# Kernel optimization log

Measured on AMD Instinct MI355X. Metric: run time of the kernel, lower is better.

## Reference

```python
import jax, jax.numpy as jnp
import numpy as np

FS = 512
SEQ_LEN = 16384
BATCH = 128
TAPS = 513  # common kernel length; per-band kernels zero-padded at the tail
N_BANDS = 20


def _design_kernels():
    """Windowed-sinc (fir1/firwin-style, hamming) bandpass kernels, tensorpac-like."""
    pha = [(f, f + 2.0) for f in np.arange(2.0, 22.0, 2.0)]    # 10 phase bands
    amp = [(f, f + 10.0) for f in np.arange(30.0, 130.0, 10.0)]  # 10 amp bands
    cycles = [3] * 10 + [6] * 10
    bands = pha + amp
    K = np.zeros((N_BANDS, TAPS), np.float32)
    for i, ((lo, hi), c) in enumerate(zip(bands, cycles)):
        order = min(int(c * FS / lo), TAPS - 1)  # fir_order ~ cycle * fs / low_hz
        taps = order + 1
        n = np.arange(taps) - (taps - 1) / 2.0
        f1, f2 = lo / FS, hi / FS
        h = 2.0 * f2 * np.sinc(2.0 * f2 * n) - 2.0 * f1 * np.sinc(2.0 * f1 * n)
        h *= np.hamming(taps)
        K[i, :taps] = h.astype(np.float32)
    return jnp.asarray(K)


def setup_inputs() -> dict:
    key = jax.random.key(0)
    x = jax.random.normal(key, (BATCH, 1, SEQ_LEN), dtype=jnp.float32)
    return {"x": x, "kernels": _design_kernels(), "padlen": TAPS - 1}


def _filtfilt_bands(x2d, kernels, P):
    """scipy.signal.filtfilt(b, 1.0, x, padlen=P) for all bands at once.
    x2d: (B, L); kernels: (nb, T) FIR taps. Odd-extension padding + lfilter_zi
    initial conditions (== constant extension of the first sample by T-1)."""
    B, L = x2d.shape
    nb, T = kernels.shape
    # odd extension: left_j = 2*x[0] - x[P-j], right_j = 2*x[-1] - x[-2-j]
    left = 2.0 * x2d[:, :1] - x2d[:, 1:P + 1][:, ::-1]
    right = 2.0 * x2d[:, -1:] - x2d[:, -P - 1:-1][:, ::-1]
    ext = jnp.concatenate([left, x2d, right], axis=1)  # (B, L + 2P)
    krev = kernels[:, ::-1][:, None, :]  # (nb, 1, T); correlation with b[::-1] == causal conv with b

    def causal_conv(sig, groups):
        # sig: (B, C, Ls); constant left-extension by T-1 (lfilter zi*x0 semantics)
        pad = jnp.repeat(sig[..., :1], T - 1, axis=-1)
        s = jnp.concatenate([pad, sig], axis=-1)
        return jax.lax.conv_general_dilated(
            s, krev, (1,), 'VALID',
            dimension_numbers=('NCW', 'OIW', 'NCW'),
            feature_group_count=groups)

    y = causal_conv(ext[:, None, :], 1)        # forward pass -> (B, nb, L+2P)
    y2 = causal_conv(y[:, :, ::-1], nb)        # backward pass (grouped, per-band)
    return y2[:, :, ::-1][:, :, P:P + L]       # un-reverse and trim padding


def reference(x, kernels, padlen):
    # x: (B, 1, L) -> (B, 1, n_bands, L)
    out = _filtfilt_bands(x[:, 0, :], kernels, padlen)
    return out[:, None, :, :]
```

## Files before the change

kernel.cpp:

```cpp
#include <hip/hip_runtime.h>

#define LSEQ   16384
#define NB     20
#define NBATCH 128
#define TAPS   513
#define CT     (2*TAPS - 1)
#define MAXSTEP 72

#define TT     2048
#define SPANE  3088
#define STRIDE 3096
#define EXTEND 16896
#define GMAX   17407

#define HDR_OFF  0
#define CS_OFF   4096
#define CSTRIDE  1040
#define ATAB_OFF 98304

typedef short  v8s  __attribute__((ext_vector_type(8)));
typedef __bf16 v8bf __attribute__((ext_vector_type(8)));
typedef float  v16f __attribute__((ext_vector_type(16)));

__device__ __forceinline__ unsigned short f2bf(float f) {
    union { float f; unsigned u; } v; v.f = f;
    return (unsigned short)((v.u + 0x7fffu + ((v.u >> 16) & 1u)) >> 16);
}

__device__ __forceinline__ v16f vzero() {
    v16f z;
    #pragma unroll
    for (int i = 0; i < 16; ++i) z[i] = 0.f;
    return z;
}

__global__ __launch_bounds__(512) void autoc_kernel(
    const float* __restrict__ Kg, float* __restrict__ Cs)
{
    __shared__ __align__(16) float kk4[4][520];
    __shared__ float ps[512];
    const int band = blockIdx.x, y = blockIdx.y;
    const int tid = threadIdx.x;
    const int rel = tid & 127, q = tid >> 7;
    const int d = 128 * y + rel;

    for (int j = tid; j < TAPS; j += 512) {
        float v = Kg[band * TAPS + j];
        kk4[0][j] = v;
        if (j >= 1) kk4[1][j - 1] = v;
        if (j >= 2) kk4[2][j - 2] = v;
        if (j >= 3) kk4[3][j - 3] = v;
    }
    if (tid < 40) {
        int c = tid / 10, t = tid % 10;
        int j = 510 + t;
        if (j >= TAPS - c && j < 520) kk4[c][j] = 0.f;
    }
    __syncthreads();

    float s = 0.f;
    if (d < CT) {
        int al = d - 512; if (al < 0) al = -al;
        const int n  = TAPS - al;
        const int c  = al & 3, sh4 = (al >> 2) << 2;
        const int nq = (((n + 3) >> 2) + 3) & ~3;
        int i0 = q * nq, i1 = i0 + nq; if (i1 > n) i1 = n;
        float s0 = 0.f, s1 = 0.f, s2 = 0.f, s3 = 0.f;
        int i = i0;
        for (; i + 3 < i1; i += 4) {
            float4 a = *(const float4*)&kk4[0][i];
            float4 b = *(const float4*)&kk4[c][i + sh4];
            s0 = fmaf(a.x, b.x, s0);
            s1 = fmaf(a.y, b.y, s1);
            s2 = fmaf(a.z, b.z, s2);
            s3 = fmaf(a.w, b.w, s3);
        }
        for (; i < i1; ++i) s0 = fmaf(kk4[0][i], kk4[c][i + sh4], s0);
        s = (s0 + s1) + (s2 + s3);
    }
    ps[tid] = s;
    __syncthreads();
    if (q == 0 && d < CT) {
        float tot = (ps[rel] + ps[rel + 128]) + (ps[rel + 256] + ps[rel + 384]);
        Cs[band * CSTRIDE + d] = tot;
    }
}

__global__ __launch_bounds__(1024) void table_kernel(
    const float* __restrict__ Cs, int2* __restrict__ hdr, short* __restrict__ atab)
{
    __shared__ float csh[CT];
    __shared__ int smin, smax, sk0, sN;
    const int band = blockIdx.x, tid = threadIdx.x;
    if (tid == 0) { smin = CT; smax = 0; }
    __syncthreads();

    const float* cb = Cs + band * CSTRIDE;
    int lmin = CT, lmax = 0;
    for (int j = tid; j < CT; j += 1024) {
        float v = cb[j];
        csh[j] = v;
        if (v != 0.f) { if (j < lmin) lmin = j; if (j > lmax) lmax = j; }
    }
    if (lmin < CT) atomicMin(&smin, lmin);
    if (lmax > 0)  atomicMax(&smax, lmax);
    __syncthreads();

    if (tid == 0) {
        int k0 = smin & ~15;
        int k1 = ((smax + 31) >> 4) << 4;
        int N  = (k1 - k0) / 16 + 1;
        int2 h; h.x = k0; h.y = N;
        hdr[band] = h;
        sk0 = k0; sN = N;
    }
    __syncthreads();

    const int k0 = sk0, N = sN;
    int nf = N + 3; if (nf > MAXSTEP) nf = MAXSTEP;
    for (int idx = tid; idx < nf * 64; idx += 1024) {
        int s = idx >> 6, lane = idx & 63;
        int m = lane & 31, kh = lane >> 5;
        int base = k0 + 16 * s + 8 * kh - m;
        v8s r;
        #pragma unroll
        for (int j = 0; j < 8; ++j) {
            int ci = base + j;
            float v = (ci >= 0 && ci < CT) ? csh[ci] : 0.f;
            r[j] = (short)f2bf(v);
        }
        *(v8s*)(atab + ((size_t)(band * MAXSTEP + s) * 64 + lane) * 8) = r;
    }
}

__global__ __launch_bounds__(256, 3) void filt_main(
    const float* __restrict__ x, const short* __restrict__ atab,
    const int2* __restrict__ hdr, float* __restrict__ out)
{
    __shared__ __align__(16) unsigned short extl[8 * STRIDE];
    const int tid = threadIdx.x;
    const int tile = blockIdx.x, grp = blockIdx.y, bg = blockIdx.z;
    const int T0 = tile * TT;

    const bool edge = (T0 < 512) || (T0 + SPANE > EXTEND);
    for (int b = 0; b < 8; ++b) {
        const float* xb = x + (size_t)(bg * 8 + b) * LSEQ;
        float x0 = 0.f, xN = 0.f;
        if (edge) { x0 = xb[0]; xN = xb[LSEQ - 1]; }
        for (int e4 = tid; e4 < SPANE / 4; e4 += 256) {
            const int e = 4 * e4;
            const int g0 = T0 + e;
            float v0, v1, v2, v3;
            if (g0 >= 512 && g0 + 4 <= EXTEND) {
                float4 xv = *(const float4*)(xb + (g0 - 512));
                v0 = xv.x; v1 = xv.y; v2 = xv.z; v3 = xv.w;
            } else {
                float vv[4];
                #pragma unroll
                for (int t = 0; t < 4; ++t) {
                    int g = g0 + t; if (g > GMAX) g = GMAX;
                    vv[t] = (g < 512)    ? 2.f * x0 - xb[512 - g]
                          : (g < EXTEND) ? xb[g - 512]
                          :                2.f * xN - xb[2 * LSEQ + 512 - 2 - g];
                }
                v0 = vv[0]; v1 = vv[1]; v2 = vv[2]; v3 = vv[3];
            }
            ushort4 qv = make_ushort4(f2bf(v0), f2bf(v1), f2bf(v2), f2bf(v3));
            *(ushort4*)&extl[b * STRIDE + e] = qv;
        }
    }
    __syncthreads();

    const int lane = tid & 63;
    const int w    = tid >> 6;
    const int n    = lane & 31, kh = lane >> 5;
    const int brow = n & 7,  tb = n >> 3;
    const unsigned short* bpb = extl + brow * STRIDE + 512 * w + 32 * tb + 8 * kh;

    const int g_start[6] = {0, 4, 8, 11, 15, 20};
    const int g_list[20] = {0,19,18,17, 1,16,15,14, 2,3,13, 4,5,6,12, 7,8,9,10,11};

    for (int bi = g_start[grp]; bi < g_start[grp + 1]; ++bi) {
        const int band = g_list[bi];
        const int2 hh = hdr[band];
        const int k0 = hh.x, N = hh.y;
        const unsigned short* bp = bpb + k0;
        const short* ap = atab + (size_t)(band * MAXSTEP) * 512 + lane * 8;

        v16f ac0 = vzero(), ac1 = vzero(), ac2 = vzero(), ac3 = vzero();
        v8bf A0 = __builtin_bit_cast(v8bf, *(const v8s*)ap);
        v8bf A1 = __builtin_bit_cast(v8bf, *(const v8s*)(ap + 512));
        v8bf A2 = __builtin_bit_cast(v8bf, *(const v8s*)(ap + 1024));
        v8bf B0 = *(const v8bf*)(bp);
        v8bf B1 = *(const v8bf*)(bp + 128);
        v8bf B2 = *(const v8bf*)(bp + 256);
        v8bf B3 = *(const v8bf*)(bp + 384);

        #pragma unroll 2
        for (int s = 0; s < N; ++s) {
            v8bf An  = __builtin_bit_cast(v8bf, *(const v8s*)(ap + (size_t)(s + 3) * 512));
            const unsigned short* bn = bp + 16 * (s + 1);
            v8bf Bn0 = *(const v8bf*)(bn);
            v8bf Bn1 = *(const v8bf*)(bn + 128);
            v8bf Bn2 = *(const v8bf*)(bn + 256);
            v8bf Bn3 = *(const v8bf*)(bn + 384);
            __builtin_amdgcn_s_setprio(1);
            ac0 = __builtin_amdgcn_mfma_f32_32x32x16_bf16(A0, B0, ac0, 0, 0, 0);
            ac1 = __builtin_amdgcn_mfma_f32_32x32x16_bf16(A0, B1, ac1, 0, 0, 0);
            ac2 = __builtin_amdgcn_mfma_f32_32x32x16_bf16(A0, B2, ac2, 0, 0, 0);
            ac3 = __builtin_amdgcn_mfma_f32_32x32x16_bf16(A0, B3, ac3, 0, 0, 0);
            __builtin_amdgcn_s_setprio(0);
            A0 = A1; A1 = A2; A2 = An;
            B0 = Bn0; B1 = Bn1; B2 = Bn2; B3 = Bn3;
        }

        float* ob = out + ((size_t)(bg * 8 + brow) * NB + band) * LSEQ
                        + T0 + 512 * w + 32 * tb + 4 * kh;
        #pragma unroll
        for (int q = 0; q < 4; ++q) {
            *(float4*)(ob +       8 * q) = make_float4(ac0[4*q], ac0[4*q+1], ac0[4*q+2], ac0[4*q+3]);
            *(float4*)(ob + 128 + 8 * q) = make_float4(ac1[4*q], ac1[4*q+1], ac1[4*q+2], ac1[4*q+3]);
            *(float4*)(ob + 256 + 8 * q) = make_float4(ac2[4*q], ac2[4*q+1], ac2[4*q+2], ac2[4*q+3]);
            *(float4*)(ob + 384 + 8 * q) = make_float4(ac3[4*q], ac3[4*q+1], ac3[4*q+2], ac3[4*q+3]);
        }
    }
}

extern "C" void kernel_launch(void* const* d_in, const int* in_sizes, int n_in,
                              void* d_out, int out_size, void* d_ws, size_t ws_size,
                              hipStream_t stream) {
    const float* x  = (const float*)d_in[0];
    const float* Kg = (const float*)d_in[1];
    float* out = (float*)d_out;

    char* wsb = (char*)d_ws;
    int2*  hdr  = (int2*)(wsb + HDR_OFF);
    float* Cs   = (float*)(wsb + CS_OFF);
    short* atab = (short*)(wsb + ATAB_OFF);

    autoc_kernel<<<dim3(NB, 9), dim3(512), 0, stream>>>(Kg, Cs);
    table_kernel<<<dim3(NB), dim3(1024), 0, stream>>>(Cs, hdr, atab);
    filt_main<<<dim3(LSEQ / TT, 5, NBATCH / 8), dim3(256), 0, stream>>>(x, atab, hdr, out);
}
```

Before: 223.9 us.

## Rebalance band groups, rotate band order per wave, prefetch next band operands

Regroups the 20 bands into five block groups with a new assignment meant to balance MFMA work per group. Each wave starts at a different band within its group, so waves in a block touch different atab regions and output rows at the same time. The first A/B operands for the next band are loaded before the current band's accumulators are stored, hiding the load latency at band boundaries. This adds register pressure from carrying extra operand registers across the store epilogue, which could hurt at the 3-blocks-per-SM bound.

```diff
diff --git a/kernel.cpp b/kernel.cpp
--- a/kernel.cpp
+++ b/kernel.cpp
@@ -177,44 +177,74 @@
     const int brow = n & 7,  tb = n >> 3;
     const unsigned short* bpb = extl + brow * STRIDE + 512 * w + 32 * tb + 8 * kh;
 
-    const int g_start[6] = {0, 4, 8, 11, 15, 20};
-    const int g_list[20] = {0,19,18,17, 1,16,15,14, 2,3,13, 4,5,6,12, 7,8,9,10,11};
-
-    for (int bi = g_start[grp]; bi < g_start[grp + 1]; ++bi) {
-        const int band = g_list[bi];
-        const int2 hh = hdr[band];
-        const int k0 = hh.x, N = hh.y;
-        const unsigned short* bp = bpb + k0;
-        const short* ap = atab + (size_t)(band * MAXSTEP) * 512 + lane * 8;
+    const int g_start[6] = {0, 2, 5, 8, 13, 20};
+    const int g_list[20] = {0,8, 1,4,17, 2,3,6, 5,7,9,10,14, 11,12,13,15,16,18,19};
+    const int gbeg = g_start[grp];
+    const int glen = g_start[grp + 1] - gbeg;
+    int rot = w; while (rot >= glen) rot -= glen;
+
+    int pos = rot;
+    int band = g_list[gbeg + pos];
+    int2 hh = hdr[band];
+    const unsigned short* bp = bpb + hh.x;
+    const short* ap = atab + (size_t)(band * MAXSTEP) * 512 + lane * 8;
+    int N = hh.y;
+    v8bf A0 = __builtin_bit_cast(v8bf, *(const v8s*)ap);
+    v8bf A1 = __builtin_bit_cast(v8bf, *(const v8s*)(ap + 512));
+    v8bf A2 = __builtin_bit_cast(v8bf, *(const v8s*)(ap + 1024));
+    v8bf B0 = *(const v8bf*)(bp);
+    v8bf B1 = *(const v8bf*)(bp + 128);
+    v8bf B2 = *(const v8bf*)(bp + 256);
+    v8bf B3 = *(const v8bf*)(bp + 384);
+
+    for (int j = 0; j < glen; ++j) {
+        const int curBand = band;
+        const int Nc = N;
+        const unsigned short* bpc = bp;
+        const short* apc = ap;
+        v8bf a0 = A0, a1 = A1, a2 = A2;
+        v8bf b0 = B0, b1 = B1, b2 = B2, b3 = B3;
+
+        const bool more = (j + 1 < glen);
+        if (more) {
+            pos = pos + 1; if (pos >= glen) pos -= glen;
+            band = g_list[gbeg + pos];
+            hh = hdr[band];
+            bp = bpb + hh.x;
+            ap = atab + (size_t)(band * MAXSTEP) * 512 + lane * 8;
+            N = hh.y;
+        }
 
         v16f ac0 = vzero(), ac1 = vzero(), ac2 = vzero(), ac3 = vzero();
-        v8bf A0 = __builtin_bit_cast(v8bf, *(const v8s*)ap);
-        v8bf A1 = __builtin_bit_cast(v8bf, *(const v8s*)(ap + 512));
-        v8bf A2 = __builtin_bit_cast(v8bf, *(const v8s*)(ap + 1024));
-        v8bf B0 = *(const v8bf*)(bp);
-        v8bf B1 = *(const v8bf*)(bp + 128);
-        v8bf B2 = *(const v8bf*)(bp + 256);
-        v8bf B3 = *(const v8bf*)(bp + 384);
-
         #pragma unroll 2
-        for (int s = 0; s < N; ++s) {
-            v8bf An  = __builtin_bit_cast(v8bf, *(const v8s*)(ap + (size_t)(s + 3) * 512));
-            const unsigned short* bn = bp + 16 * (s + 1);
+        for (int s = 0; s < Nc; ++s) {
+            v8bf An  = __builtin_bit_cast(v8bf, *(const v8s*)(apc + (size_t)(s + 3) * 512));
+            const unsigned short* bn = bpc + 16 * (s + 1);
             v8bf Bn0 = *(const v8bf*)(bn);
             v8bf Bn1 = *(const v8bf*)(bn + 128);
             v8bf Bn2 = *(const v8bf*)(bn + 256);
             v8bf Bn3 = *(const v8bf*)(bn + 384);
             __builtin_amdgcn_s_setprio(1);
-            ac0 = __builtin_amdgcn_mfma_f32_32x32x16_bf16(A0, B0, ac0, 0, 0, 0);
-            ac1 = __builtin_amdgcn_mfma_f32_32x32x16_bf16(A0, B1, ac1, 0, 0, 0);
-            ac2 = __builtin_amdgcn_mfma_f32_32x32x16_bf16(A0, B2, ac2, 0, 0, 0);
-            ac3 = __builtin_amdgcn_mfma_f32_32x32x16_bf16(A0, B3, ac3, 0, 0, 0);
+            ac0 = __builtin_amdgcn_mfma_f32_32x32x16_bf16(a0, b0, ac0, 0, 0, 0);
+            ac1 = __builtin_amdgcn_mfma_f32_32x32x16_bf16(a0, b1, ac1, 0, 0, 0);
+            ac2 = __builtin_amdgcn_mfma_f32_32x32x16_bf16(a0, b2, ac2, 0, 0, 0);
+            ac3 = __builtin_amdgcn_mfma_f32_32x32x16_bf16(a0, b3, ac3, 0, 0, 0);
             __builtin_amdgcn_s_setprio(0);
-            A0 = A1; A1 = A2; A2 = An;
-            B0 = Bn0; B1 = Bn1; B2 = Bn2; B3 = Bn3;
-        }
-
-        float* ob = out + ((size_t)(bg * 8 + brow) * NB + band) * LSEQ
+            a0 = a1; a1 = a2; a2 = An;
+            b0 = Bn0; b1 = Bn1; b2 = Bn2; b3 = Bn3;
+        }
+
+        if (more) {
+            A0 = __builtin_bit_cast(v8bf, *(const v8s*)ap);
+            A1 = __builtin_bit_cast(v8bf, *(const v8s*)(ap + 512));
+            A2 = __builtin_bit_cast(v8bf, *(const v8s*)(ap + 1024));
+            B0 = *(const v8bf*)(bp);
+            B1 = *(const v8bf*)(bp + 128);
+            B2 = *(const v8bf*)(bp + 256);
+            B3 = *(const v8bf*)(bp + 384);
+        }
+
+        float* ob = out + ((size_t)(bg * 8 + brow) * NB + curBand) * LSEQ
                         + T0 + 512 * w + 32 * tb + 4 * kh;
         #pragma unroll
         for (int q = 0; q < 4; ++q) {
```

After: 224.3 us. Within noise of the previous version (+0.1%).

## Reuse sliding LDS B-window registers across MFMA steps with swizzled LDS layout

Applied to the files above, without the earlier changes.

The four accumulators now cover adjacent 32-sample column blocks, so their B operands overlap by 32 samples. An 8-register rotating window of B fragments is kept, and each step issues one new LDS load where the old code issued four. The extl layout gets an XOR swizzle to reduce bank conflicts, and the band-to-block grouping is rebalanced. In exchange the loop is padded to a multiple of 8 steps, which lengthens the A-table (MAXSTEP raised to 80) and adds some zero-padded wasted MFMAs.

```diff
diff --git a/kernel.cpp b/kernel.cpp
--- a/kernel.cpp
+++ b/kernel.cpp
@@ -5,7 +5,7 @@
 #define NBATCH 128
 #define TAPS   513
 #define CT     (2*TAPS - 1)
-#define MAXSTEP 72
+#define MAXSTEP 80
 
 #define TT     2048
 #define SPANE  3088
@@ -32,6 +32,11 @@
     #pragma unroll
     for (int i = 0; i < 16; ++i) z[i] = 0.f;
     return z;
+}
+
+__device__ __forceinline__ v8bf ld_swz(const unsigned short* base, int ldw) {
+    int ph = ldw ^ (((ldw >> 6) & 3) << 2);
+    return __builtin_bit_cast(v8bf, *(const v8s*)((const char*)base + (size_t)ph * 4));
 }
 
 __global__ __launch_bounds__(512) void autoc_kernel(
@@ -117,7 +122,8 @@
     __syncthreads();
 
     const int k0 = sk0, N = sN;
-    int nf = N + 3; if (nf > MAXSTEP) nf = MAXSTEP;
+    const int Np = (N + 7) & ~7;
+    int nf = Np + 3; if (nf > MAXSTEP) nf = MAXSTEP;
     for (int idx = tid; idx < nf * 64; idx += 1024) {
         int s = idx >> 6, lane = idx & 63;
         int m = lane & 31, kh = lane >> 5;
@@ -166,7 +172,9 @@
                 v0 = vv[0]; v1 = vv[1]; v2 = vv[2]; v3 = vv[3];
             }
             ushort4 qv = make_ushort4(f2bf(v0), f2bf(v1), f2bf(v2), f2bf(v3));
-            *(ushort4*)&extl[b * STRIDE + e] = qv;
+            int ldw = (b * STRIDE + e) >> 1;
+            int ph  = ldw ^ (((ldw >> 6) & 3) << 2);
+            *(ushort4*)((char*)extl + (size_t)ph * 4) = qv;
         }
     }
     __syncthreads();
@@ -175,53 +183,54 @@
     const int w    = tid >> 6;
     const int n    = lane & 31, kh = lane >> 5;
     const int brow = n & 7,  tb = n >> 3;
-    const unsigned short* bpb = extl + brow * STRIDE + 512 * w + 32 * tb + 8 * kh;
-
-    const int g_start[6] = {0, 4, 8, 11, 15, 20};
-    const int g_list[20] = {0,19,18,17, 1,16,15,14, 2,3,13, 4,5,6,12, 7,8,9,10,11};
+    const int laneDW = brow * (STRIDE / 2) + 256 * w + 64 * tb + 4 * kh;
+
+    const int g_start[6] = {0, 2, 5, 8, 14, 20};
+    const int g_list[20] = {0,5, 1,4,14, 2,3,6, 7,8,9,10,15,16, 11,12,13,17,18,19};
 
     for (int bi = g_start[grp]; bi < g_start[grp + 1]; ++bi) {
         const int band = g_list[bi];
         const int2 hh = hdr[band];
         const int k0 = hh.x, N = hh.y;
-        const unsigned short* bp = bpb + k0;
+        const int Np   = (N + 7) & ~7;
+        const int umax = N + 5;
+        const int bdw  = laneDW + (k0 >> 1);
         const short* ap = atab + (size_t)(band * MAXSTEP) * 512 + lane * 8;
 
         v16f ac0 = vzero(), ac1 = vzero(), ac2 = vzero(), ac3 = vzero();
         v8bf A0 = __builtin_bit_cast(v8bf, *(const v8s*)ap);
         v8bf A1 = __builtin_bit_cast(v8bf, *(const v8s*)(ap + 512));
         v8bf A2 = __builtin_bit_cast(v8bf, *(const v8s*)(ap + 1024));
-        v8bf B0 = *(const v8bf*)(bp);
-        v8bf B1 = *(const v8bf*)(bp + 128);
-        v8bf B2 = *(const v8bf*)(bp + 256);
-        v8bf B3 = *(const v8bf*)(bp + 384);
-
-        #pragma unroll 2
-        for (int s = 0; s < N; ++s) {
-            v8bf An  = __builtin_bit_cast(v8bf, *(const v8s*)(ap + (size_t)(s + 3) * 512));
-            const unsigned short* bn = bp + 16 * (s + 1);
-            v8bf Bn0 = *(const v8bf*)(bn);
-            v8bf Bn1 = *(const v8bf*)(bn + 128);
-            v8bf Bn2 = *(const v8bf*)(bn + 256);
-            v8bf Bn3 = *(const v8bf*)(bn + 384);
-            __builtin_amdgcn_s_setprio(1);
-            ac0 = __builtin_amdgcn_mfma_f32_32x32x16_bf16(A0, B0, ac0, 0, 0, 0);
-            ac1 = __builtin_amdgcn_mfma_f32_32x32x16_bf16(A0, B1, ac1, 0, 0, 0);
-            ac2 = __builtin_amdgcn_mfma_f32_32x32x16_bf16(A0, B2, ac2, 0, 0, 0);
-            ac3 = __builtin_amdgcn_mfma_f32_32x32x16_bf16(A0, B3, ac3, 0, 0, 0);
-            __builtin_amdgcn_s_setprio(0);
-            A0 = A1; A1 = A2; A2 = An;
-            B0 = Bn0; B1 = Bn1; B2 = Bn2; B3 = Bn3;
-        }
+        v8bf W[8];
+        #pragma unroll
+        for (int t = 0; t < 8; ++t) W[t] = ld_swz(extl, bdw + 8 * t);
+
+        #define FSTEP(c) { \
+            v8bf An = __builtin_bit_cast(v8bf, *(const v8s*)(ap + (size_t)(sb + (c) + 3) * 512)); \
+            __builtin_amdgcn_s_setprio(1); \
+            ac0 = __builtin_amdgcn_mfma_f32_32x32x16_bf16(A0, W[((c)+0)&7], ac0, 0, 0, 0); \
+            ac1 = __builtin_amdgcn_mfma_f32_32x32x16_bf16(A0, W[((c)+2)&7], ac1, 0, 0, 0); \
+            ac2 = __builtin_amdgcn_mfma_f32_32x32x16_bf16(A0, W[((c)+4)&7], ac2, 0, 0, 0); \
+            ac3 = __builtin_amdgcn_mfma_f32_32x32x16_bf16(A0, W[((c)+6)&7], ac3, 0, 0, 0); \
+            __builtin_amdgcn_s_setprio(0); \
+            A0 = A1; A1 = A2; A2 = An; \
+            int u = sb + (c) + 8; if (u > umax) u = umax; \
+            W[(c) & 7] = ld_swz(extl, bdw + 8 * u); \
+        }
+        for (int sb = 0; sb < Np; sb += 8) {
+            FSTEP(0) FSTEP(1) FSTEP(2) FSTEP(3)
+            FSTEP(4) FSTEP(5) FSTEP(6) FSTEP(7)
+        }
+        #undef FSTEP
 
         float* ob = out + ((size_t)(bg * 8 + brow) * NB + band) * LSEQ
-                        + T0 + 512 * w + 32 * tb + 4 * kh;
+                        + T0 + 512 * w + 128 * tb + 4 * kh;
         #pragma unroll
         for (int q = 0; q < 4; ++q) {
-            *(float4*)(ob +       8 * q) = make_float4(ac0[4*q], ac0[4*q+1], ac0[4*q+2], ac0[4*q+3]);
-            *(float4*)(ob + 128 + 8 * q) = make_float4(ac1[4*q], ac1[4*q+1], ac1[4*q+2], ac1[4*q+3]);
-            *(float4*)(ob + 256 + 8 * q) = make_float4(ac2[4*q], ac2[4*q+1], ac2[4*q+2], ac2[4*q+3]);
-            *(float4*)(ob + 384 + 8 * q) = make_float4(ac3[4*q], ac3[4*q+1], ac3[4*q+2], ac3[4*q+3]);
+            *(float4*)(ob +      8 * q) = make_float4(ac0[4*q], ac0[4*q+1], ac0[4*q+2], ac0[4*q+3]);
+            *(float4*)(ob + 32 + 8 * q) = make_float4(ac1[4*q], ac1[4*q+1], ac1[4*q+2], ac1[4*q+3]);
+            *(float4*)(ob + 64 + 8 * q) = make_float4(ac2[4*q], ac2[4*q+1], ac2[4*q+2], ac2[4*q+3]);
+            *(float4*)(ob + 96 + 8 * q) = make_float4(ac3[4*q], ac3[4*q+1], ac3[4*q+2], ac3[4*q+3]);
         }
     }
 }
```

Result: no change. 225.5 us (+0.7%).

## Retile filter MFMA: 4 batch rows x 4096 samples per block, rebalance band groups

Applied to the files above, without the earlier changes.

The main filter kernel's tile shape changes from 8 batch rows by 2048 samples to 4 batch rows by 4096 samples per block. Each MFMA N-column now maps to 4 rows with 8 sub-offsets, and each wave covers 1024 samples. The band-to-group assignment is rebalanced and MAXSTEP is raised. B-fragment software prefetch is dropped in favour of in-loop LDS loads. The intent is less halo overhead per tile and better load balance across groups, at the cost of a larger LDS footprint and possibly more exposed LDS latency.

```diff
diff --git a/kernel.cpp b/kernel.cpp
--- a/kernel.cpp
+++ b/kernel.cpp
@@ -5,11 +5,12 @@
 #define NBATCH 128
 #define TAPS   513
 #define CT     (2*TAPS - 1)
-#define MAXSTEP 72
-
-#define TT     2048
-#define SPANE  3088
-#define STRIDE 3096
+#define MAXSTEP 80
+
+#define TT     4096
+#define NROW   4
+#define SPANE  5136
+#define STRIDE 5144
 #define EXTEND 16896
 #define GMAX   17407
 
@@ -137,14 +138,14 @@
     const float* __restrict__ x, const short* __restrict__ atab,
     const int2* __restrict__ hdr, float* __restrict__ out)
 {
-    __shared__ __align__(16) unsigned short extl[8 * STRIDE];
+    __shared__ __align__(16) unsigned short extl[NROW * STRIDE];
     const int tid = threadIdx.x;
     const int tile = blockIdx.x, grp = blockIdx.y, bg = blockIdx.z;
     const int T0 = tile * TT;
 
     const bool edge = (T0 < 512) || (T0 + SPANE > EXTEND);
-    for (int b = 0; b < 8; ++b) {
-        const float* xb = x + (size_t)(bg * 8 + b) * LSEQ;
+    for (int b = 0; b < NROW; ++b) {
+        const float* xb = x + (size_t)(bg * NROW + b) * LSEQ;
         float x0 = 0.f, xN = 0.f;
         if (edge) { x0 = xb[0]; xN = xb[LSEQ - 1]; }
         for (int e4 = tid; e4 < SPANE / 4; e4 += 256) {
@@ -174,11 +175,11 @@
     const int lane = tid & 63;
     const int w    = tid >> 6;
     const int n    = lane & 31, kh = lane >> 5;
-    const int brow = n & 7,  tb = n >> 3;
-    const unsigned short* bpb = extl + brow * STRIDE + 512 * w + 32 * tb + 8 * kh;
-
-    const int g_start[6] = {0, 4, 8, 11, 15, 20};
-    const int g_list[20] = {0,19,18,17, 1,16,15,14, 2,3,13, 4,5,6,12, 7,8,9,10,11};
+    const int b    = n >> 3, sub = n & 7;
+    const unsigned short* bpb = extl + b * STRIDE + 1024 * w + 32 * sub + 8 * kh;
+
+    const int g_start[6] = {0, 2, 5, 8, 14, 20};
+    const int g_list[20] = {0,5, 1,4,14, 2,3,6, 7,8,9,10,15,16, 11,12,13,17,18,19};
 
     for (int bi = g_start[grp]; bi < g_start[grp + 1]; ++bi) {
         const int band = g_list[bi];
@@ -191,19 +192,15 @@
         v8bf A0 = __builtin_bit_cast(v8bf, *(const v8s*)ap);
         v8bf A1 = __builtin_bit_cast(v8bf, *(const v8s*)(ap + 512));
         v8bf A2 = __builtin_bit_cast(v8bf, *(const v8s*)(ap + 1024));
-        v8bf B0 = *(const v8bf*)(bp);
-        v8bf B1 = *(const v8bf*)(bp + 128);
-        v8bf B2 = *(const v8bf*)(bp + 256);
-        v8bf B3 = *(const v8bf*)(bp + 384);
 
         #pragma unroll 2
         for (int s = 0; s < N; ++s) {
-            v8bf An  = __builtin_bit_cast(v8bf, *(const v8s*)(ap + (size_t)(s + 3) * 512));
-            const unsigned short* bn = bp + 16 * (s + 1);
-            v8bf Bn0 = *(const v8bf*)(bn);
-            v8bf Bn1 = *(const v8bf*)(bn + 128);
-            v8bf Bn2 = *(const v8bf*)(bn + 256);
-            v8bf Bn3 = *(const v8bf*)(bn + 384);
+            v8bf An = __builtin_bit_cast(v8bf, *(const v8s*)(ap + (size_t)(s + 3) * 512));
+            const unsigned short* bn = bp + 16 * s;
+            v8bf B0 = *(const v8bf*)(bn);
+            v8bf B1 = *(const v8bf*)(bn + 256);
+            v8bf B2 = *(const v8bf*)(bn + 512);
+            v8bf B3 = *(const v8bf*)(bn + 768);
             __builtin_amdgcn_s_setprio(1);
             ac0 = __builtin_amdgcn_mfma_f32_32x32x16_bf16(A0, B0, ac0, 0, 0, 0);
             ac1 = __builtin_amdgcn_mfma_f32_32x32x16_bf16(A0, B1, ac1, 0, 0, 0);
@@ -211,17 +208,16 @@
             ac3 = __builtin_amdgcn_mfma_f32_32x32x16_bf16(A0, B3, ac3, 0, 0, 0);
             __builtin_amdgcn_s_setprio(0);
             A0 = A1; A1 = A2; A2 = An;
-            B0 = Bn0; B1 = Bn1; B2 = Bn2; B3 = Bn3;
-        }
-
-        float* ob = out + ((size_t)(bg * 8 + brow) * NB + band) * LSEQ
-                        + T0 + 512 * w + 32 * tb + 4 * kh;
+        }
+
+        float* ob = out + ((size_t)(bg * NROW + b) * NB + band) * LSEQ
+                        + T0 + 1024 * w + 32 * sub + 4 * kh;
         #pragma unroll
         for (int q = 0; q < 4; ++q) {
             *(float4*)(ob +       8 * q) = make_float4(ac0[4*q], ac0[4*q+1], ac0[4*q+2], ac0[4*q+3]);
-            *(float4*)(ob + 128 + 8 * q) = make_float4(ac1[4*q], ac1[4*q+1], ac1[4*q+2], ac1[4*q+3]);
-            *(float4*)(ob + 256 + 8 * q) = make_float4(ac2[4*q], ac2[4*q+1], ac2[4*q+2], ac2[4*q+3]);
-            *(float4*)(ob + 384 + 8 * q) = make_float4(ac3[4*q], ac3[4*q+1], ac3[4*q+2], ac3[4*q+3]);
+            *(float4*)(ob + 256 + 8 * q) = make_float4(ac1[4*q], ac1[4*q+1], ac1[4*q+2], ac1[4*q+3]);
+            *(float4*)(ob + 512 + 8 * q) = make_float4(ac2[4*q], ac2[4*q+1], ac2[4*q+2], ac2[4*q+3]);
+            *(float4*)(ob + 768 + 8 * q) = make_float4(ac3[4*q], ac3[4*q+1], ac3[4*q+2], ac3[4*q+3]);
         }
     }
 }
@@ -240,5 +236,5 @@
 
     autoc_kernel<<<dim3(NB, 9), dim3(512), 0, stream>>>(Kg, Cs);
     table_kernel<<<dim3(NB), dim3(1024), 0, stream>>>(Cs, hdr, atab);
-    filt_main<<<dim3(LSEQ / TT, 5, NBATCH / 8), dim3(256), 0, stream>>>(x, atab, hdr, out);
-}
+    filt_main<<<dim3(LSEQ / TT, 5, NBATCH / NROW), dim3(256), 0, stream>>>(x, atab, hdr, out);
+}
```

After: 220.4 us. Within noise of the previous version (-1.6%).
